# Performance work log

Measured on AMD Instinct MI355X. Metric: run time of the kernel, lower is better.

The kernel has to match this reference:

```python
import jax, jax.numpy as jnp
import numpy as np

N_NODES = 100000
N_EDGES = 1600000
IN_F, HID_F, OUT_F = 128, 128, 64


def setup_inputs() -> dict:
    key = jax.random.key(0)
    ks = jax.random.split(key, 10)
    x = jax.random.normal(ks[0], (N_NODES, IN_F), dtype=jnp.float32)
    adj_row = jax.random.randint(ks[1], (N_EDGES,), 0, N_NODES, dtype=jnp.int64)
    adj_col = jax.random.randint(ks[2], (N_EDGES,), 0, N_NODES, dtype=jnp.int64)
    adj_val = jax.random.uniform(ks[3], (N_EDGES,), dtype=jnp.float32)
    # layer weights (xavier-normal-ish scale), stored as [in, out]
    def w(k, fin, fout):
        return jax.random.normal(k, (fin, fout), dtype=jnp.float32) * jnp.sqrt(2.0 / (fin + fout))
    return {
        "x": x, "adj_row": adj_row, "adj_col": adj_col, "adj_val": adj_val,
        "W0": w(ks[4], IN_F, HID_F), "b0": jnp.zeros((HID_F,), jnp.float32),
        "W1": w(ks[5], HID_F, HID_F), "b1": jnp.zeros((HID_F,), jnp.float32),
        "W2": w(ks[6], HID_F, OUT_F), "b2": jnp.zeros((OUT_F,), jnp.float32),
    }


def _spmm(adj_row, adj_col, adj_val, h):
    # sparse [N,N] @ dense [N,F]: gather source rows, scale, scatter-add to dest
    msgs = adj_val[:, None] * h[adj_col]            # [E, F]
    return jax.ops.segment_sum(msgs, adj_row, num_segments=N_NODES)


def reference(x, adj_row, adj_col, adj_val, W0, b0, W1, b1, W2, b2):
    h = x
    params = [(W0, b0), (W1, b1), (W2, b2)]
    n_layers = len(params)
    for i, (W, b) in enumerate(params):
        h = h @ W + b                               # Linear
        h = _spmm(adj_row, adj_col, adj_val, h)     # torch.sparse.mm(adj, h)
        if i != n_layers - 1:
            h = jax.nn.relu(h)                      # activation on hidden layers only
    return h


if __name__ == "__main__":
    out = reference(**setup_inputs())
    print(out.shape)
```

## Files before the change

### kernel.cpp

```cpp
#include <hip/hip_runtime.h>
#include <hip/hip_bf16.h>

#define N_NODES 100000
#define N_EDGES 1600000

#define BIN_SHIFT 9
#define NBIN 196
#define NBLK 256
#define CHUNK 6250
#define SCAN_N (NBIN * NBLK)

typedef __attribute__((ext_vector_type(8))) short bf16x8;
typedef __attribute__((ext_vector_type(4))) float f32x4;

__device__ inline unsigned short f2bf(float f) {
    union { float f; unsigned u; } v; v.f = f;
    unsigned r = v.u + 0x7FFF + ((v.u >> 16) & 1);
    return (unsigned short)(r >> 16);
}
__device__ inline float bf2f(unsigned short h) {
    union { unsigned u; float f; } v; v.u = ((unsigned)h) << 16;
    return v.f;
}


__global__ __launch_bounds__(256) void p1_bincnt(const int* __restrict__ row,
                                                 int* __restrict__ cnt) {
    __shared__ int h[NBIN];
    for (int i = threadIdx.x; i < NBIN; i += 256) h[i] = 0;
    __syncthreads();
    int base = blockIdx.x * CHUNK;
    int end = base + CHUNK; if (end > N_EDGES) end = N_EDGES;
    for (int i = base + threadIdx.x; i < end; i += 256)
        atomicAdd(&h[row[i] >> BIN_SHIFT], 1);
    __syncthreads();
    for (int b = threadIdx.x; b < NBIN; b += 256)
        cnt[b * NBLK + blockIdx.x] = h[b];
}

__global__ __launch_bounds__(1024) void p2_scan(const int* __restrict__ cnt,
                                                int* __restrict__ base,
                                                int* __restrict__ rp) {
    __shared__ int s[1024];
    int t = threadIdx.x;
    const int per = SCAN_N / 1024;
    int lo = t * per, hi = lo + per;
    int sum = 0;
    for (int i = lo; i < hi; ++i) sum += cnt[i];
    s[t] = sum;
    __syncthreads();
    for (int off = 1; off < 1024; off <<= 1) {
        int v = (t >= off) ? s[t - off] : 0;
        __syncthreads();
        s[t] += v;
        __syncthreads();
    }
    int run = s[t] - sum;
    for (int i = lo; i < hi; ++i) { int c = cnt[i]; base[i] = run; run += c; }
    if (t == 0) rp[N_NODES] = N_EDGES;
}

__global__ __launch_bounds__(256) void p3_partition(const int* __restrict__ row,
                                                    const int* __restrict__ col,
                                                    const float* __restrict__ val,
                                                    const int* __restrict__ base,
                                                    int2* __restrict__ bout) {
    __shared__ int cur[NBIN];
    for (int i = threadIdx.x; i < NBIN; i += 256)
        cur[i] = base[i * NBLK + blockIdx.x];
    __syncthreads();
    int lo = blockIdx.x * CHUNK;
    int end = lo + CHUNK; if (end > N_EDGES) end = N_EDGES;
    for (int i = lo + threadIdx.x; i < end; i += 256) {
        int r = row[i];
        int b = r >> BIN_SHIFT;
        int p = atomicAdd(&cur[b], 1);
        int2 rec;
        rec.x = col[i] | ((r & 511) << 17);
        rec.y = __float_as_int(val[i]);
        bout[p] = rec;
    }
}


__global__ __launch_bounds__(256) void p4_binscatter(const int* __restrict__ base,
                                                     const int2* __restrict__ bin_in,
                                                     int* __restrict__ rp,
                                                     int2* __restrict__ erec) {
    __shared__ int cnt[4096];
    __shared__ int part[256];
    const int b = blockIdx.x;
    const int t = threadIdx.x;
    const int lo = base[b * NBLK];
    const int hi = (b + 1 < NBIN) ? base[(b + 1) * NBLK] : N_EDGES;

    for (int i = t; i < 4096; i += 256) cnt[i] = 0;
    __syncthreads();
    for (int e = lo + t; e < hi; e += 256) {
        int2 q = bin_in[e];
        int rl = (unsigned)q.x >> 17;
        int ck = (q.x & 0x1FFFF) >> 14;
        atomicAdd(&cnt[(rl << 3) | ck], 1);
    }
    __syncthreads();

    int local[16]; int sum = 0;
    #pragma unroll
    for (int k = 0; k < 16; ++k) { local[k] = cnt[t * 16 + k]; sum += local[k]; }
    part[t] = sum;
    __syncthreads();
    for (int off = 1; off < 256; off <<= 1) {
        int v = (t >= off) ? part[t - off] : 0;
        __syncthreads();
        part[t] += v;
        __syncthreads();
    }
    int run = part[t] - sum;
    #pragma unroll
    for (int k = 0; k < 16; ++k) { int c = local[k]; cnt[t * 16 + k] = run; run += c; }

    const int rowbase = b << BIN_SHIFT;
    int r0 = rowbase + 2 * t, r1 = rowbase + 2 * t + 1;
    if (r0 < N_NODES) rp[r0] = lo + cnt[t * 16];
    if (r1 < N_NODES) rp[r1] = lo + cnt[t * 16 + 8];
    __syncthreads();

    for (int e = lo + t; e < hi; e += 256) {
        int2 q = bin_in[e];
        int rl = (unsigned)q.x >> 17;
        int c = q.x & 0x1FFFF;
        int p = lo + atomicAdd(&cnt[(rl << 3) | (c >> 14)], 1);
        int2 rec;
        rec.x = c;
        rec.y = q.y;
        erec[p] = rec;
    }
}


__global__ __launch_bounds__(256) void pack_all(const float* __restrict__ W0,
                                                const float* __restrict__ W1,
                                                const float* __restrict__ W2,
                                                unsigned short* __restrict__ Bp0,
                                                unsigned short* __restrict__ Bp1,
                                                unsigned short* __restrict__ Bp2) {
    int idx = blockIdx.x * 256 + threadIdx.x;
    const float* W; unsigned short* Bp; int fout, li;
    if (idx < 16384)      { W = W0; Bp = Bp0; fout = 128; li = idx; }
    else if (idx < 32768) { W = W1; Bp = Bp1; fout = 128; li = idx - 16384; }
    else                  { W = W2; Bp = Bp2; fout = 64;  li = idx - 32768; }
    int j = li & 7, lane = (li >> 3) & 63, kb = (li >> 9) & 3, nt = li >> 11;
    int k = kb * 32 + (lane >> 4) * 8 + j;
    int col = nt * 16 + (lane & 15);
    Bp[li] = f2bf(W[k * fout + col]);
}


template<int FOUT, bool AF32>
__global__ __launch_bounds__(256) void gemm_mfma(const void* __restrict__ Xv,
                                                 const unsigned short* __restrict__ Bp,
                                                 const float* __restrict__ bias,
                                                 unsigned short* __restrict__ Y, int n) {
    const int wave = threadIdx.x >> 6;
    const int lane = threadIdx.x & 63;
    const int l15 = lane & 15, kg = lane >> 4;
    const int nbase = blockIdx.y * 64;
    const int rowTile = blockIdx.x * 128 + wave * 32;

    int r0 = rowTile + l15;      if (r0 >= n) r0 = n - 1;
    int r1 = rowTile + 16 + l15; if (r1 >= n) r1 = n - 1;

    bf16x8 a0[4], a1[4];
    if constexpr (AF32) {
        const float* x0 = (const float*)Xv + (size_t)r0 * 128 + kg * 8;
        const float* x1 = (const float*)Xv + (size_t)r1 * 128 + kg * 8;
        #pragma unroll
        for (int kb = 0; kb < 4; ++kb) {
            float4 u = *reinterpret_cast<const float4*>(x0 + kb * 32);
            float4 v = *reinterpret_cast<const float4*>(x0 + kb * 32 + 4);
            a0[kb] = (bf16x8){(short)f2bf(u.x), (short)f2bf(u.y), (short)f2bf(u.z), (short)f2bf(u.w),
                              (short)f2bf(v.x), (short)f2bf(v.y), (short)f2bf(v.z), (short)f2bf(v.w)};
            float4 p = *reinterpret_cast<const float4*>(x1 + kb * 32);
            float4 q = *reinterpret_cast<const float4*>(x1 + kb * 32 + 4);
            a1[kb] = (bf16x8){(short)f2bf(p.x), (short)f2bf(p.y), (short)f2bf(p.z), (short)f2bf(p.w),
                              (short)f2bf(q.x), (short)f2bf(q.y), (short)f2bf(q.z), (short)f2bf(q.w)};
        }
    } else {
        const bf16x8* x0 = reinterpret_cast<const bf16x8*>((const unsigned short*)Xv + (size_t)r0 * 128 + kg * 8);
        const bf16x8* x1 = reinterpret_cast<const bf16x8*>((const unsigned short*)Xv + (size_t)r1 * 128 + kg * 8);
        #pragma unroll
        for (int kb = 0; kb < 4; ++kb) { a0[kb] = x0[kb * 4]; a1[kb] = x1[kb * 4]; }
    }

    f32x4 c0[4], c1[4];
    #pragma unroll
    for (int t = 0; t < 4; ++t) {
        c0[t] = (f32x4){0.f, 0.f, 0.f, 0.f};
        c1[t] = (f32x4){0.f, 0.f, 0.f, 0.f};
    }

    const bf16x8* bpv = reinterpret_cast<const bf16x8*>(Bp);
    #pragma unroll
    for (int nt = 0; nt < 4; ++nt) {
        int ntAbs = (nbase >> 4) + nt;
        const bf16x8* bp = bpv + (size_t)(ntAbs * 4) * 64 + lane;
        #pragma unroll
        for (int kb = 0; kb < 4; ++kb) {
            bf16x8 b = bp[kb * 64];
            c0[nt] = __builtin_amdgcn_mfma_f32_16x16x32_bf16(a0[kb], b, c0[nt], 0, 0, 0);
            c1[nt] = __builtin_amdgcn_mfma_f32_16x16x32_bf16(a1[kb], b, c1[nt], 0, 0, 0);
        }
    }

    #pragma unroll
    for (int nt = 0; nt < 4; ++nt) {
        int col = nbase + nt * 16 + l15;
        float bv = bias[col];
        int rb = rowTile + kg * 4;
        #pragma unroll
        for (int j = 0; j < 4; ++j) {
            int ra = rb + j;
            if (ra < n) Y[(size_t)ra * FOUT + col] = f2bf(c0[nt][j] + bv);
            int rc = rb + 16 + j;
            if (rc < n) Y[(size_t)rc * FOUT + col] = f2bf(c1[nt][j] + bv);
        }
    }
}


__global__ __launch_bounds__(256) void spmm_mid(const int* __restrict__ rp,
                                                const int2* __restrict__ erec,
                                                const unsigned* __restrict__ G,
                                                unsigned* __restrict__ Y, int n) {
    int node = blockIdx.x * 4 + (threadIdx.x >> 6);
    if (node >= n) return;
    int lane = threadIdx.x & 63;
    int e0 = rp[node], e1 = rp[node + 1];
    float a0 = 0.f, a1 = 0.f;
    const unsigned* Gf = G + lane;
    while (e0 < e1) {
        int take = e1 - e0; if (take > 64) take = 64;
        int2 rec = erec[e0 + (lane < take ? lane : take - 1)];
        int i = 0;
        for (; i + 8 <= take; i += 8) {
            unsigned g[8]; float v[8];
            #pragma unroll
            for (int j = 0; j < 8; ++j) {
                int c = __builtin_amdgcn_readlane(rec.x, i + j);
                v[j] = __int_as_float(__builtin_amdgcn_readlane(rec.y, i + j));
                g[j] = Gf[(size_t)c * 64];
            }
            #pragma unroll
            for (int j = 0; j < 8; ++j) {
                a0 += v[j] * bf2f((unsigned short)g[j]);
                a1 += v[j] * bf2f((unsigned short)(g[j] >> 16));
            }
        }
        for (; i < take; ++i) {
            int c = __builtin_amdgcn_readlane(rec.x, i);
            float v = __int_as_float(__builtin_amdgcn_readlane(rec.y, i));
            unsigned g = Gf[(size_t)c * 64];
            a0 += v * bf2f((unsigned short)g);
            a1 += v * bf2f((unsigned short)(g >> 16));
        }
        e0 += take;
    }
    a0 = fmaxf(a0, 0.f); a1 = fmaxf(a1, 0.f);
    Y[(size_t)node * 64 + lane] = (unsigned)f2bf(a0) | ((unsigned)f2bf(a1) << 16);
}


__global__ __launch_bounds__(256) void spmm_last(const int* __restrict__ rp,
                                                 const int2* __restrict__ erec,
                                                 const unsigned short* __restrict__ G,
                                                 float* __restrict__ out, int n) {
    int node = blockIdx.x * 4 + (threadIdx.x >> 6);
    if (node >= n) return;
    int lane = threadIdx.x & 63;
    int eg = lane >> 3, fg = lane & 7;
    int e0 = rp[node], e1 = rp[node + 1];
    float acc[8] = {0.f, 0.f, 0.f, 0.f, 0.f, 0.f, 0.f, 0.f};
    while (e0 < e1) {
        int take = e1 - e0; if (take > 64) take = 64;
        int2 rec = erec[e0 + (lane < take ? lane : take - 1)];
        for (int r = 0; r < take; r += 16) {
            uint4 d[2]; float vv[2];
            #pragma unroll
            for (int s = 0; s < 2; ++s) {
                int idx = r + s * 8 + eg;
                bool ok = idx < take;
                int src = ok ? idx : take - 1;
                int c = __shfl(rec.x, src);
                float v = __int_as_float(__shfl(rec.y, src));
                vv[s] = ok ? v : 0.f;
                d[s] = *reinterpret_cast<const uint4*>(G + (size_t)c * 64 + fg * 8);
            }
            #pragma unroll
            for (int s = 0; s < 2; ++s) {
                unsigned w0 = d[s].x, w1 = d[s].y, w2 = d[s].z, w3 = d[s].w;
                acc[0] += vv[s] * bf2f((unsigned short)w0);
                acc[1] += vv[s] * bf2f((unsigned short)(w0 >> 16));
                acc[2] += vv[s] * bf2f((unsigned short)w1);
                acc[3] += vv[s] * bf2f((unsigned short)(w1 >> 16));
                acc[4] += vv[s] * bf2f((unsigned short)w2);
                acc[5] += vv[s] * bf2f((unsigned short)(w2 >> 16));
                acc[6] += vv[s] * bf2f((unsigned short)w3);
                acc[7] += vv[s] * bf2f((unsigned short)(w3 >> 16));
            }
        }
        e0 += take;
    }
    #pragma unroll
    for (int k = 0; k < 8; ++k) {
        acc[k] += __shfl_xor(acc[k], 8);
        acc[k] += __shfl_xor(acc[k], 16);
        acc[k] += __shfl_xor(acc[k], 32);
    }
    if (eg == 0) {
        float4 oA = {acc[0], acc[1], acc[2], acc[3]};
        float4 oB = {acc[4], acc[5], acc[6], acc[7]};
        float4* o = reinterpret_cast<float4*>(out + (size_t)node * 64 + fg * 8);
        o[0] = oA;
        o[1] = oB;
    }
}


extern "C" void kernel_launch(void* const* d_in, const int* in_sizes, int n_in,
                              void* d_out, int out_size, void* d_ws, size_t ws_size,
                              hipStream_t stream) {
    const float* x    = (const float*)d_in[0];
    const int*   arow = (const int*)d_in[1];
    const int*   acol = (const int*)d_in[2];
    const float* aval = (const float*)d_in[3];
    const float* W0   = (const float*)d_in[4];
    const float* b0   = (const float*)d_in[5];
    const float* W1   = (const float*)d_in[6];
    const float* b1   = (const float*)d_in[7];
    const float* W2   = (const float*)d_in[8];
    const float* b2   = (const float*)d_in[9];
    float* out = (float*)d_out;

    unsigned short* hlin = (unsigned short*)d_ws;
    unsigned short* hact = hlin + (size_t)N_NODES * 128;
    unsigned short* Bp0  = hact + (size_t)N_NODES * 128;
    unsigned short* Bp1  = Bp0 + 16384;
    unsigned short* Bp2  = Bp1 + 16384;
    int* cnt  = (int*)(Bp2 + 8192);
    int* base = cnt + SCAN_N;
    int* rp   = base + SCAN_N;
    int2* bin_in = (int2*)(rp + N_NODES + 2);
    int2* erec   = bin_in + N_EDGES;

    p1_bincnt<<<NBLK, 256, 0, stream>>>(arow, cnt);
    p2_scan<<<1, 1024, 0, stream>>>(cnt, base, rp);
    p3_partition<<<NBLK, 256, 0, stream>>>(arow, acol, aval, base, bin_in);
    p4_binscatter<<<NBIN, 256, 0, stream>>>(base, bin_in, rp, erec);

    pack_all<<<160, 256, 0, stream>>>(W0, W1, W2, Bp0, Bp1, Bp2);

    dim3 gemm_grid((N_NODES + 127) / 128, 2);
    dim3 gemm_grid2((N_NODES + 127) / 128, 1);
    int spmm_grid = (N_NODES + 3) / 4;

    gemm_mfma<128, true><<<gemm_grid, 256, 0, stream>>>(x, Bp0, b0, hlin, N_NODES);
    spmm_mid<<<spmm_grid, 256, 0, stream>>>(rp, erec, (const unsigned*)hlin, (unsigned*)hact, N_NODES);
    gemm_mfma<128, false><<<gemm_grid, 256, 0, stream>>>(hact, Bp1, b1, hlin, N_NODES);
    spmm_mid<<<spmm_grid, 256, 0, stream>>>(rp, erec, (const unsigned*)hlin, (unsigned*)hact, N_NODES);
    gemm_mfma<64, false><<<gemm_grid2, 256, 0, stream>>>(hact, Bp2, b2, hlin, N_NODES);
    spmm_last<<<spmm_grid, 256, 0, stream>>>(rp, erec, hlin, out, N_NODES);
}
```

Before: 303.5 us.

## Column-bucket edges per row and process SpMM node groups bucket-by-bucket

The edge sort now splits each row's edges into 13 column buckets of 8192 columns and records per-row bucket offsets in a new rpb array. A new mid-layer SpMM kernel gives each block 68 nodes (17 per wave) and stages their edge records in LDS. It sweeps the buckets in order so concurrent waves gather from a narrow, L2-sized slice of the feature matrix. This aims to cut gather misses, but it adds rpb writes and reads, and each wave handles one edge at a time with a dependent load. That lowers the number of gathers in flight compared with the old 8-wide readlane batching.

```diff
diff --git a/kernel.cpp b/kernel.cpp
--- a/kernel.cpp
+++ b/kernel.cpp
@@ -9,6 +9,12 @@
 #define NBLK 256
 #define CHUNK 6250
 #define SCAN_N (NBIN * NBLK)
+
+#define BK_SHIFT 13
+#define NBKT 13
+#define NPB 68
+#define NPW 17
+#define ECAP 2048
 
 typedef __attribute__((ext_vector_type(8))) short bf16x8;
 typedef __attribute__((ext_vector_type(4))) float f32x4;
@@ -86,27 +92,28 @@
 __global__ __launch_bounds__(256) void p4_binscatter(const int* __restrict__ base,
                                                      const int2* __restrict__ bin_in,
                                                      int* __restrict__ rp,
+                                                     int* __restrict__ rpb,
                                                      int2* __restrict__ erec) {
-    __shared__ int cnt[4096];
+    __shared__ int cnt[512 * NBKT];
     __shared__ int part[256];
     const int b = blockIdx.x;
     const int t = threadIdx.x;
     const int lo = base[b * NBLK];
     const int hi = (b + 1 < NBIN) ? base[(b + 1) * NBLK] : N_EDGES;
 
-    for (int i = t; i < 4096; i += 256) cnt[i] = 0;
+    for (int i = t; i < 512 * NBKT; i += 256) cnt[i] = 0;
     __syncthreads();
     for (int e = lo + t; e < hi; e += 256) {
         int2 q = bin_in[e];
         int rl = (unsigned)q.x >> 17;
-        int ck = (q.x & 0x1FFFF) >> 14;
-        atomicAdd(&cnt[(rl << 3) | ck], 1);
-    }
-    __syncthreads();
-
-    int local[16]; int sum = 0;
-    #pragma unroll
-    for (int k = 0; k < 16; ++k) { local[k] = cnt[t * 16 + k]; sum += local[k]; }
+        int ck = (q.x & 0x1FFFF) >> BK_SHIFT;
+        atomicAdd(&cnt[rl * NBKT + ck], 1);
+    }
+    __syncthreads();
+
+    int local[2 * NBKT]; int sum = 0;
+    #pragma unroll
+    for (int k = 0; k < 2 * NBKT; ++k) { local[k] = cnt[t * 2 * NBKT + k]; sum += local[k]; }
     part[t] = sum;
     __syncthreads();
     for (int off = 1; off < 256; off <<= 1) {
@@ -117,19 +124,27 @@
     }
     int run = part[t] - sum;
     #pragma unroll
-    for (int k = 0; k < 16; ++k) { int c = local[k]; cnt[t * 16 + k] = run; run += c; }
+    for (int k = 0; k < 2 * NBKT; ++k) { int c = local[k]; cnt[t * 2 * NBKT + k] = run; run += c; }
 
     const int rowbase = b << BIN_SHIFT;
-    int r0 = rowbase + 2 * t, r1 = rowbase + 2 * t + 1;
-    if (r0 < N_NODES) rp[r0] = lo + cnt[t * 16];
-    if (r1 < N_NODES) rp[r1] = lo + cnt[t * 16 + 8];
+    int r0 = rowbase + 2 * t, r1 = r0 + 1;
+    if (r0 < N_NODES) {
+        rp[r0] = lo + cnt[t * 2 * NBKT];
+        #pragma unroll
+        for (int k = 0; k < NBKT; ++k) rpb[r0 * NBKT + k] = lo + cnt[t * 2 * NBKT + k];
+    }
+    if (r1 < N_NODES) {
+        rp[r1] = lo + cnt[t * 2 * NBKT + NBKT];
+        #pragma unroll
+        for (int k = 0; k < NBKT; ++k) rpb[r1 * NBKT + k] = lo + cnt[t * 2 * NBKT + NBKT + k];
+    }
     __syncthreads();
 
     for (int e = lo + t; e < hi; e += 256) {
         int2 q = bin_in[e];
         int rl = (unsigned)q.x >> 17;
         int c = q.x & 0x1FFFF;
-        int p = lo + atomicAdd(&cnt[(rl << 3) | (c >> 14)], 1);
+        int p = lo + atomicAdd(&cnt[rl * NBKT + (c >> BK_SHIFT)], 1);
         int2 rec;
         rec.x = c;
         rec.y = q.y;
@@ -228,45 +243,66 @@
 }
 
 
-__global__ __launch_bounds__(256) void spmm_mid(const int* __restrict__ rp,
-                                                const int2* __restrict__ erec,
-                                                const unsigned* __restrict__ G,
-                                                unsigned* __restrict__ Y, int n) {
-    int node = blockIdx.x * 4 + (threadIdx.x >> 6);
-    if (node >= n) return;
-    int lane = threadIdx.x & 63;
-    int e0 = rp[node], e1 = rp[node + 1];
-    float a0 = 0.f, a1 = 0.f;
+__global__ __launch_bounds__(256, 6) void spmm_mid_p(const int* __restrict__ rp,
+                                                     const int* __restrict__ rpb,
+                                                     const int2* __restrict__ erec,
+                                                     const unsigned* __restrict__ G,
+                                                     unsigned* __restrict__ Y, int n) {
+    __shared__ int2 lds_e[ECAP];
+    __shared__ int rpb_l[NPB * NBKT];
+    __shared__ int rp_l[NPB + 1];
+    const int node0 = blockIdx.x * NPB;
+    int nEnd = node0 + NPB; if (nEnd > n) nEnd = n;
+    const int nLoc = nEnd - node0;
+    const int t = threadIdx.x;
+
+    for (int i = t; i <= NPB; i += 256) {
+        int nd = node0 + i; if (nd > n) nd = n;
+        rp_l[i] = rp[nd];
+    }
+    for (int i = t; i < nLoc * NBKT; i += 256)
+        rpb_l[i] = rpb[node0 * NBKT + i];
+    const int lo = rp[node0];
+    {
+        int m = rp[nEnd < n ? nEnd : n] - lo; if (m > ECAP) m = ECAP;
+        for (int i = t; i < m; i += 256) lds_e[i] = erec[lo + i];
+    }
+    __syncthreads();
+
+    const int wave = t >> 6, lane = t & 63;
+    const int nb = wave * NPW;
     const unsigned* Gf = G + lane;
-    while (e0 < e1) {
-        int take = e1 - e0; if (take > 64) take = 64;
-        int2 rec = erec[e0 + (lane < take ? lane : take - 1)];
-        int i = 0;
-        for (; i + 8 <= take; i += 8) {
-            unsigned g[8]; float v[8];
-            #pragma unroll
-            for (int j = 0; j < 8; ++j) {
-                int c = __builtin_amdgcn_readlane(rec.x, i + j);
-                v[j] = __int_as_float(__builtin_amdgcn_readlane(rec.y, i + j));
-                g[j] = Gf[(size_t)c * 64];
+    float a0[NPW], a1[NPW];
+    #pragma unroll
+    for (int ni = 0; ni < NPW; ++ni) { a0[ni] = 0.f; a1[ni] = 0.f; }
+
+    for (int b = 0; b < NBKT; ++b) {
+        #pragma unroll
+        for (int ni = 0; ni < NPW; ++ni) {
+            int ln = nb + ni;
+            if (ln < nLoc) {
+                int s = rpb_l[ln * NBKT + b];
+                int e = (b == NBKT - 1) ? rp_l[ln + 1] : rpb_l[ln * NBKT + b + 1];
+                for (int i = s; i < e; ++i) {
+                    int idx = i - lo;
+                    int2 q = (idx < ECAP) ? lds_e[idx] : erec[i];
+                    float v = __int_as_float(q.y);
+                    unsigned g = Gf[(size_t)q.x * 64];
+                    a0[ni] += v * bf2f((unsigned short)g);
+                    a1[ni] += v * bf2f((unsigned short)(g >> 16));
+                }
             }
-            #pragma unroll
-            for (int j = 0; j < 8; ++j) {
-                a0 += v[j] * bf2f((unsigned short)g[j]);
-                a1 += v[j] * bf2f((unsigned short)(g[j] >> 16));
-            }
-        }
-        for (; i < take; ++i) {
-            int c = __builtin_amdgcn_readlane(rec.x, i);
-            float v = __int_as_float(__builtin_amdgcn_readlane(rec.y, i));
-            unsigned g = Gf[(size_t)c * 64];
-            a0 += v * bf2f((unsigned short)g);
-            a1 += v * bf2f((unsigned short)(g >> 16));
-        }
-        e0 += take;
-    }
-    a0 = fmaxf(a0, 0.f); a1 = fmaxf(a1, 0.f);
-    Y[(size_t)node * 64 + lane] = (unsigned)f2bf(a0) | ((unsigned)f2bf(a1) << 16);
+        }
+    }
+
+    #pragma unroll
+    for (int ni = 0; ni < NPW; ++ni) {
+        int ln = nb + ni;
+        if (ln < nLoc) {
+            float f0 = fmaxf(a0[ni], 0.f), f1 = fmaxf(a1[ni], 0.f);
+            Y[(size_t)(node0 + ln) * 64 + lane] = (unsigned)f2bf(f0) | ((unsigned)f2bf(f1) << 16);
+        }
+    }
 }
 
 
@@ -349,24 +385,26 @@
     int* cnt  = (int*)(Bp2 + 8192);
     int* base = cnt + SCAN_N;
     int* rp   = base + SCAN_N;
-    int2* bin_in = (int2*)(rp + N_NODES + 2);
+    int* rpb  = rp + N_NODES + 2;
+    int2* bin_in = (int2*)(rpb + (size_t)N_NODES * NBKT + 2);
     int2* erec   = bin_in + N_EDGES;
 
     p1_bincnt<<<NBLK, 256, 0, stream>>>(arow, cnt);
     p2_scan<<<1, 1024, 0, stream>>>(cnt, base, rp);
     p3_partition<<<NBLK, 256, 0, stream>>>(arow, acol, aval, base, bin_in);
-    p4_binscatter<<<NBIN, 256, 0, stream>>>(base, bin_in, rp, erec);
+    p4_binscatter<<<NBIN, 256, 0, stream>>>(base, bin_in, rp, rpb, erec);
 
     pack_all<<<160, 256, 0, stream>>>(W0, W1, W2, Bp0, Bp1, Bp2);
 
     dim3 gemm_grid((N_NODES + 127) / 128, 2);
     dim3 gemm_grid2((N_NODES + 127) / 128, 1);
+    int pgrid = (N_NODES + NPB - 1) / NPB;
     int spmm_grid = (N_NODES + 3) / 4;
 
     gemm_mfma<128, true><<<gemm_grid, 256, 0, stream>>>(x, Bp0, b0, hlin, N_NODES);
-    spmm_mid<<<spmm_grid, 256, 0, stream>>>(rp, erec, (const unsigned*)hlin, (unsigned*)hact, N_NODES);
+    spmm_mid_p<<<pgrid, 256, 0, stream>>>(rp, rpb, erec, (const unsigned*)hlin, (unsigned*)hact, N_NODES);
     gemm_mfma<128, false><<<gemm_grid, 256, 0, stream>>>(hact, Bp1, b1, hlin, N_NODES);
-    spmm_mid<<<spmm_grid, 256, 0, stream>>>(rp, erec, (const unsigned*)hlin, (unsigned*)hact, N_NODES);
+    spmm_mid_p<<<pgrid, 256, 0, stream>>>(rp, rpb, erec, (const unsigned*)hlin, (unsigned*)hact, N_NODES);
     gemm_mfma<64, false><<<gemm_grid2, 256, 0, stream>>>(hact, Bp2, b2, hlin, N_NODES);
     spmm_last<<<spmm_grid, 256, 0, stream>>>(rp, erec, hlin, out, N_NODES);
 }
```

Result: slower. 466.3 us (+53.6%).

## Pack edge records into 32-bit words with bf16 values and fuse weight packing

Applied to the files above, without the earlier changes.

Edge records are compressed from an int2 (column, fp32 value) to a single 32-bit word holding a 17-bit column and a 15-bit bf16 value. This halves the index stream read by every SpMM. The per-row column-chunk sub-sort in the bin scatter is dropped, simplifying that kernel, and weight packing is merged into the bin-count launch to save a launch. In exchange, edge weights lose precision to bf16 with the sign bit dropped, which relies on values being non-negative, and gather locality within a row may get worse.

```diff
diff --git a/kernel.cpp b/kernel.cpp
--- a/kernel.cpp
+++ b/kernel.cpp
@@ -24,18 +24,36 @@
 }
 
 
-__global__ __launch_bounds__(256) void p1_bincnt(const int* __restrict__ row,
-                                                 int* __restrict__ cnt) {
-    __shared__ int h[NBIN];
-    for (int i = threadIdx.x; i < NBIN; i += 256) h[i] = 0;
-    __syncthreads();
-    int base = blockIdx.x * CHUNK;
-    int end = base + CHUNK; if (end > N_EDGES) end = N_EDGES;
-    for (int i = base + threadIdx.x; i < end; i += 256)
-        atomicAdd(&h[row[i] >> BIN_SHIFT], 1);
-    __syncthreads();
-    for (int b = threadIdx.x; b < NBIN; b += 256)
-        cnt[b * NBLK + blockIdx.x] = h[b];
+__global__ __launch_bounds__(256) void p1_pack(const int* __restrict__ row,
+                                               int* __restrict__ cnt,
+                                               const float* __restrict__ W0,
+                                               const float* __restrict__ W1,
+                                               const float* __restrict__ W2,
+                                               unsigned short* __restrict__ Bp0,
+                                               unsigned short* __restrict__ Bp1,
+                                               unsigned short* __restrict__ Bp2) {
+    if (blockIdx.x < NBLK) {
+        __shared__ int h[NBIN];
+        for (int i = threadIdx.x; i < NBIN; i += 256) h[i] = 0;
+        __syncthreads();
+        int base = blockIdx.x * CHUNK;
+        int end = base + CHUNK; if (end > N_EDGES) end = N_EDGES;
+        for (int i = base + threadIdx.x; i < end; i += 256)
+            atomicAdd(&h[row[i] >> BIN_SHIFT], 1);
+        __syncthreads();
+        for (int b = threadIdx.x; b < NBIN; b += 256)
+            cnt[b * NBLK + blockIdx.x] = h[b];
+    } else {
+        int idx = (blockIdx.x - NBLK) * 256 + threadIdx.x;
+        const float* W; unsigned short* Bp; int fout, li;
+        if (idx < 16384)      { W = W0; Bp = Bp0; fout = 128; li = idx; }
+        else if (idx < 32768) { W = W1; Bp = Bp1; fout = 128; li = idx - 16384; }
+        else                  { W = W2; Bp = Bp2; fout = 64;  li = idx - 32768; }
+        int j = li & 7, lane = (li >> 3) & 63, kb = (li >> 9) & 3, nt = li >> 11;
+        int k = kb * 32 + (lane >> 4) * 8 + j;
+        int col = nt * 16 + (lane & 15);
+        Bp[li] = f2bf(W[k * fout + col]);
+    }
 }
 
 __global__ __launch_bounds__(1024) void p2_scan(const int* __restrict__ cnt,
@@ -86,73 +104,47 @@
 __global__ __launch_bounds__(256) void p4_binscatter(const int* __restrict__ base,
                                                      const int2* __restrict__ bin_in,
                                                      int* __restrict__ rp,
-                                                     int2* __restrict__ erec) {
-    __shared__ int cnt[4096];
+                                                     unsigned* __restrict__ erec) {
+    __shared__ int cnt[512];
     __shared__ int part[256];
     const int b = blockIdx.x;
     const int t = threadIdx.x;
     const int lo = base[b * NBLK];
     const int hi = (b + 1 < NBIN) ? base[(b + 1) * NBLK] : N_EDGES;
 
-    for (int i = t; i < 4096; i += 256) cnt[i] = 0;
-    __syncthreads();
+    cnt[t] = 0; cnt[t + 256] = 0;
+    __syncthreads();
+    for (int e = lo + t; e < hi; e += 256)
+        atomicAdd(&cnt[(unsigned)bin_in[e].x >> 17], 1);
+    __syncthreads();
+
+    int s0 = cnt[2 * t], s1 = cnt[2 * t + 1];
+    int tsum = s0 + s1;
+    part[t] = tsum;
+    __syncthreads();
+    for (int off = 1; off < 256; off <<= 1) {
+        int v = (t >= off) ? part[t - off] : 0;
+        __syncthreads();
+        part[t] += v;
+        __syncthreads();
+    }
+    int run = part[t] - tsum;
+    cnt[2 * t] = run;
+    cnt[2 * t + 1] = run + s0;
+
+    const int rowbase = b << BIN_SHIFT;
+    int r0 = rowbase + 2 * t, r1 = rowbase + 2 * t + 1;
+    if (r0 < N_NODES) rp[r0] = lo + run;
+    if (r1 < N_NODES) rp[r1] = lo + run + s0;
+    __syncthreads();
+
     for (int e = lo + t; e < hi; e += 256) {
         int2 q = bin_in[e];
         int rl = (unsigned)q.x >> 17;
-        int ck = (q.x & 0x1FFFF) >> 14;
-        atomicAdd(&cnt[(rl << 3) | ck], 1);
-    }
-    __syncthreads();
-
-    int local[16]; int sum = 0;
-    #pragma unroll
-    for (int k = 0; k < 16; ++k) { local[k] = cnt[t * 16 + k]; sum += local[k]; }
-    part[t] = sum;
-    __syncthreads();
-    for (int off = 1; off < 256; off <<= 1) {
-        int v = (t >= off) ? part[t - off] : 0;
-        __syncthreads();
-        part[t] += v;
-        __syncthreads();
-    }
-    int run = part[t] - sum;
-    #pragma unroll
-    for (int k = 0; k < 16; ++k) { int c = local[k]; cnt[t * 16 + k] = run; run += c; }
-
-    const int rowbase = b << BIN_SHIFT;
-    int r0 = rowbase + 2 * t, r1 = rowbase + 2 * t + 1;
-    if (r0 < N_NODES) rp[r0] = lo + cnt[t * 16];
-    if (r1 < N_NODES) rp[r1] = lo + cnt[t * 16 + 8];
-    __syncthreads();
-
-    for (int e = lo + t; e < hi; e += 256) {
-        int2 q = bin_in[e];
-        int rl = (unsigned)q.x >> 17;
-        int c = q.x & 0x1FFFF;
-        int p = lo + atomicAdd(&cnt[(rl << 3) | (c >> 14)], 1);
-        int2 rec;
-        rec.x = c;
-        rec.y = q.y;
-        erec[p] = rec;
-    }
-}
-
-
-__global__ __launch_bounds__(256) void pack_all(const float* __restrict__ W0,
-                                                const float* __restrict__ W1,
-                                                const float* __restrict__ W2,
-                                                unsigned short* __restrict__ Bp0,
-                                                unsigned short* __restrict__ Bp1,
-                                                unsigned short* __restrict__ Bp2) {
-    int idx = blockIdx.x * 256 + threadIdx.x;
-    const float* W; unsigned short* Bp; int fout, li;
-    if (idx < 16384)      { W = W0; Bp = Bp0; fout = 128; li = idx; }
-    else if (idx < 32768) { W = W1; Bp = Bp1; fout = 128; li = idx - 16384; }
-    else                  { W = W2; Bp = Bp2; fout = 64;  li = idx - 32768; }
-    int j = li & 7, lane = (li >> 3) & 63, kb = (li >> 9) & 3, nt = li >> 11;
-    int k = kb * 32 + (lane >> 4) * 8 + j;
-    int col = nt * 16 + (lane & 15);
-    Bp[li] = f2bf(W[k * fout + col]);
+        int p = lo + atomicAdd(&cnt[rl], 1);
+        unsigned c = (unsigned)(q.x & 0x1FFFF);
+        erec[p] = (c << 15) | ((unsigned)f2bf(__int_as_float(q.y)) & 0x7FFFu);
+    }
 }
 
 
@@ -229,7 +221,7 @@
 
 
 __global__ __launch_bounds__(256) void spmm_mid(const int* __restrict__ rp,
-                                                const int2* __restrict__ erec,
+                                                const unsigned* __restrict__ erec,
                                                 const unsigned* __restrict__ G,
                                                 unsigned* __restrict__ Y, int n) {
     int node = blockIdx.x * 4 + (threadIdx.x >> 6);
@@ -240,15 +232,15 @@
     const unsigned* Gf = G + lane;
     while (e0 < e1) {
         int take = e1 - e0; if (take > 64) take = 64;
-        int2 rec = erec[e0 + (lane < take ? lane : take - 1)];
+        unsigned rec = erec[e0 + (lane < take ? lane : take - 1)];
         int i = 0;
         for (; i + 8 <= take; i += 8) {
             unsigned g[8]; float v[8];
             #pragma unroll
             for (int j = 0; j < 8; ++j) {
-                int c = __builtin_amdgcn_readlane(rec.x, i + j);
-                v[j] = __int_as_float(__builtin_amdgcn_readlane(rec.y, i + j));
-                g[j] = Gf[(size_t)c * 64];
+                unsigned q = __builtin_amdgcn_readlane(rec, i + j);
+                v[j] = __uint_as_float((q & 0x7FFFu) << 16);
+                g[j] = Gf[(size_t)(q >> 15) * 64];
             }
             #pragma unroll
             for (int j = 0; j < 8; ++j) {
@@ -257,9 +249,9 @@
             }
         }
         for (; i < take; ++i) {
-            int c = __builtin_amdgcn_readlane(rec.x, i);
-            float v = __int_as_float(__builtin_amdgcn_readlane(rec.y, i));
-            unsigned g = Gf[(size_t)c * 64];
+            unsigned q = __builtin_amdgcn_readlane(rec, i);
+            float v = __uint_as_float((q & 0x7FFFu) << 16);
+            unsigned g = Gf[(size_t)(q >> 15) * 64];
             a0 += v * bf2f((unsigned short)g);
             a1 += v * bf2f((unsigned short)(g >> 16));
         }
@@ -271,7 +263,7 @@
 
 
 __global__ __launch_bounds__(256) void spmm_last(const int* __restrict__ rp,
-                                                 const int2* __restrict__ erec,
+                                                 const unsigned* __restrict__ erec,
                                                  const unsigned short* __restrict__ G,
                                                  float* __restrict__ out, int n) {
     int node = blockIdx.x * 4 + (threadIdx.x >> 6);
@@ -282,7 +274,7 @@
     float acc[8] = {0.f, 0.f, 0.f, 0.f, 0.f, 0.f, 0.f, 0.f};
     while (e0 < e1) {
         int take = e1 - e0; if (take > 64) take = 64;
-        int2 rec = erec[e0 + (lane < take ? lane : take - 1)];
+        unsigned rec = erec[e0 + (lane < take ? lane : take - 1)];
         for (int r = 0; r < take; r += 16) {
             uint4 d[2]; float vv[2];
             #pragma unroll
@@ -290,10 +282,10 @@
                 int idx = r + s * 8 + eg;
                 bool ok = idx < take;
                 int src = ok ? idx : take - 1;
-                int c = __shfl(rec.x, src);
-                float v = __int_as_float(__shfl(rec.y, src));
+                unsigned q = __shfl(rec, src);
+                float v = __uint_as_float((q & 0x7FFFu) << 16);
                 vv[s] = ok ? v : 0.f;
-                d[s] = *reinterpret_cast<const uint4*>(G + (size_t)c * 64 + fg * 8);
+                d[s] = *reinterpret_cast<const uint4*>(G + (size_t)(q >> 15) * 64 + fg * 8);
             }
             #pragma unroll
             for (int s = 0; s < 2; ++s) {
@@ -350,14 +342,12 @@
     int* base = cnt + SCAN_N;
     int* rp   = base + SCAN_N;
     int2* bin_in = (int2*)(rp + N_NODES + 2);
-    int2* erec   = bin_in + N_EDGES;
-
-    p1_bincnt<<<NBLK, 256, 0, stream>>>(arow, cnt);
+    unsigned* erec = (unsigned*)(bin_in + N_EDGES);
+
+    p1_pack<<<NBLK + 160, 256, 0, stream>>>(arow, cnt, W0, W1, W2, Bp0, Bp1, Bp2);
     p2_scan<<<1, 1024, 0, stream>>>(cnt, base, rp);
     p3_partition<<<NBLK, 256, 0, stream>>>(arow, acol, aval, base, bin_in);
     p4_binscatter<<<NBIN, 256, 0, stream>>>(base, bin_in, rp, erec);
-
-    pack_all<<<160, 256, 0, stream>>>(W0, W1, W2, Bp0, Bp1, Bp2);
 
     dim3 gemm_grid((N_NODES + 127) / 128, 2);
     dim3 gemm_grid2((N_NODES + 127) / 128, 1);
```

Result: faster. 295.3 us (-2.7%).
